# Optimization experiments

Hardware: AMD Instinct MI355X
Metric: run time of the kernel (lower is better)

## Reference

```python
import jax, jax.numpy as jnp
import numpy as np

B, S, DIM = 8, 1, 2048
H = 16
QLR, KVLR = 1536, 512
DN, DR, DV = 128, 64, 128      # qk_nope, qk_rope, v head dims
START = 8191                    # start_pos; end_pos = START + S = 8192
EPS = 1e-6
SCALE = (DN + DR) ** -0.5


def _rms(x, w):
    # F.rms_norm: x / sqrt(mean(x^2)+eps) * w
    return x * w * jax.lax.rsqrt(jnp.mean(jnp.square(x), axis=-1, keepdims=True) + EPS)


def _rope(x, cos, sin):
    # x: [..., r]; consecutive pairs (x0,x1) treated as complex, multiplied by cos+i*sin
    xr, xi = x[..., 0::2], x[..., 1::2]
    out_r = xr * cos - xi * sin
    out_i = xr * sin + xi * cos
    return jnp.stack([out_r, out_i], axis=-1).reshape(x.shape)


def setup_inputs() -> dict:
    key = jax.random.key(0)
    ks = jax.random.split(key, 12)
    # rotary tables for the single decode position
    inv_freq = 1.0 / (10000.0 ** (np.arange(0, DR, 2, dtype=np.float32) / DR))  # [DR/2]
    pos = np.arange(START, START + S, dtype=np.float32)[:, None]                # [S,1]
    ang = pos * inv_freq[None, :]                                               # [S, DR/2]
    return {
        "x": jax.random.normal(ks[0], (B, S, DIM), jnp.float32),
        "start_pos": START,
        "freqs_cos": jnp.asarray(np.cos(ang)),
        "freqs_sin": jnp.asarray(np.sin(ang)),
        "kv_cache_prefix": jax.random.normal(ks[1], (B, START, KVLR), jnp.float32),
        "pe_cache_prefix": jax.random.normal(ks[2], (B, START, DR), jnp.float32),
        "wq_a_w": jax.random.normal(ks[3], (QLR, DIM), jnp.float32) * 0.02,
        "wq_a_b": jnp.zeros((QLR,), jnp.float32),
        "q_norm_w": jnp.ones((QLR,), jnp.float32),
        "wq_b_w": jax.random.normal(ks[4], (H * (DN + DR), QLR), jnp.float32) * 0.02,
        "wq_b_b": jnp.zeros((H * (DN + DR),), jnp.float32),
        "wkv_a_w": jax.random.normal(ks[5], (KVLR + DR, DIM), jnp.float32) * 0.02,
        "wkv_a_b": jnp.zeros((KVLR + DR,), jnp.float32),
        "kv_norm_w": jnp.ones((KVLR,), jnp.float32),
        "wkv_b_w": jax.random.normal(ks[6], (H * (DN + DV), KVLR), jnp.float32) * 0.02,
        "wo_w": jax.random.normal(ks[7], (DIM, H * DV), jnp.float32) * 0.02,
        "wo_b": jnp.zeros((DIM,), jnp.float32),
    }


def reference(x, start_pos, freqs_cos, freqs_sin, kv_cache_prefix, pe_cache_prefix,
              wq_a_w, wq_a_b, q_norm_w, wq_b_w, wq_b_b,
              wkv_a_w, wkv_a_b, kv_norm_w, wkv_b_w, wo_w, wo_b):
    b, s, _ = x.shape
    # low-rank query projection
    q = _rms(x @ wq_a_w.T + wq_a_b, q_norm_w) @ wq_b_w.T + wq_b_b
    q = q.reshape(b, s, H, DN + DR)
    q_nope, q_pe = q[..., :DN], q[..., DN:]
    cos = freqs_cos[None, :, None, :]  # [1,s,1,DR/2]
    sin = freqs_sin[None, :, None, :]
    q_pe = _rope(q_pe, cos, sin)
    # compressed KV + rope key branch
    kvpe = x @ wkv_a_w.T + wkv_a_b               # [b,s,KVLR+DR]
    kv, k_pe = kvpe[..., :KVLR], kvpe[..., KVLR:]
    k_pe = _rope(k_pe[:, :, None, :], cos, sin)[:, :, 0, :]
    # weight absorption: project q_nope into latent space through wkv_b's K-part
    wkv_b = wkv_b_w.reshape(H, DN + DV, KVLR)
    q_abs = jnp.einsum('bshd,hdc->bshc', q_nope, wkv_b[:, :DN])
    # append current step to caches
    kv_cache = jnp.concatenate([kv_cache_prefix, _rms(kv, kv_norm_w)], axis=1)  # [b,t,KVLR]
    pe_cache = jnp.concatenate([pe_cache_prefix, k_pe], axis=1)                 # [b,t,DR]
    # attention in latent space (seqlen=1 decode -> no causal mask needed)
    scores = (jnp.einsum('bshc,btc->bsht', q_abs, kv_cache)
              + jnp.einsum('bshr,btr->bsht', q_pe, pe_cache)) * SCALE
    attn = jax.nn.softmax(scores.astype(jnp.float32), axis=-1).astype(x.dtype)
    out = jnp.einsum('bsht,btc->bshc', attn, kv_cache)
    out = jnp.einsum('bshc,hdc->bshd', out, wkv_b[:, DN:])  # V-part of wkv_b
    return out.reshape(b, s, H * DV) @ wo_w.T + wo_b
```

## Files before the change

kernel.cpp:

```cpp
#include <hip/hip_runtime.h>
#include <math.h>

namespace {
constexpr int B_   = 8;
constexpr int DIM_ = 2048;
constexpr int H_   = 16;
constexpr int QLR_ = 1536;
constexpr int KVLR_= 512;
constexpr int DN_  = 128;
constexpr int DR_  = 64;
constexpr int DV_  = 128;
constexpr int TPRE_= 8191;
constexpr int CE_  = 576;
constexpr int NCH_ = 32;
constexpr int CT_  = 256;
constexpr int TS_  = 32;
constexpr int PSTR_= 20;
constexpr float EPS_ = 1e-6f;
constexpr float SCALE_ = 0.07216878364870322f;

constexpr size_t WS_QLAT  = 0;
constexpr size_t WS_KVPE  = WS_QLAT  + (size_t)B_*QLR_;
constexpr size_t WS_KVNEW = WS_KVPE  + (size_t)B_*CE_;
constexpr size_t WS_PENEW = WS_KVNEW + (size_t)B_*KVLR_;
constexpr size_t WS_QRS   = WS_PENEW + (size_t)B_*DR_;
constexpr size_t WS_QNOPE = WS_QRS   + (size_t)B_;
constexpr size_t WS_QT    = WS_QNOPE + (size_t)B_*H_*DN_;
constexpr size_t WS_MLOC  = WS_QT    + (size_t)B_*CE_*H_;
constexpr size_t WS_LLOC  = WS_MLOC  + (size_t)B_*H_*NCH_;
constexpr size_t WS_OUT2  = WS_LLOC  + (size_t)B_*H_*NCH_;
constexpr size_t WS_OPART = WS_OUT2  + (size_t)B_*DIM_;
}

__device__ __forceinline__ void gload16(const float* src, float* ldsDst) {
  __builtin_amdgcn_global_load_lds((const __attribute__((address_space(1))) void*)src,
                                   (__attribute__((address_space(3))) void*)ldsDst,
                                   16, 0, 0);
}

__device__ __forceinline__ float rsum16(float v) {
  int x = __float_as_int(v);
  v += __int_as_float(__builtin_amdgcn_update_dpp(0, x, 0xB1, 0xF, 0xF, true));
  x = __float_as_int(v);
  v += __int_as_float(__builtin_amdgcn_update_dpp(0, x, 0x4E, 0xF, 0xF, true));
  x = __float_as_int(v);
  v += __int_as_float(__builtin_amdgcn_update_dpp(0, x, 0x141, 0xF, 0xF, true));
  x = __float_as_int(v);
  v += __int_as_float(__builtin_amdgcn_update_dpp(0, x, 0x140, 0xF, 0xF, true));
  return v;
}

__global__ __launch_bounds__(256) void mla_k1(const float* __restrict__ x,
                                              const float* __restrict__ wqa,
                                              const float* __restrict__ bqa,
                                              const float* __restrict__ wkva,
                                              const float* __restrict__ bkva,
                                              float* __restrict__ ws) {
  const int w = threadIdx.x >> 6, l = threadIdx.x & 63;
  const int r = blockIdx.x * 4 + w;
  const float* W; const float* bias; float* out; int rr; int ostride;
  if (r < QLR_) { W = wqa;  bias = bqa;  out = ws + WS_QLAT; rr = r;        ostride = QLR_; }
  else          { W = wkva; bias = bkva; out = ws + WS_KVPE; rr = r - QLR_; ostride = CE_;  }
  const float4* wp = (const float4*)(W + (size_t)rr * DIM_);
  const float4* x4 = (const float4*)x;
  float4 wv[8];
#pragma unroll
  for (int j = 0; j < 8; ++j) wv[j] = wp[l + 64 * j];
  float acc[B_];
#pragma unroll
  for (int b = 0; b < B_; ++b) acc[b] = 0.f;
#pragma unroll
  for (int b = 0; b < B_; ++b) {
#pragma unroll
    for (int j = 0; j < 8; ++j) {
      const float4 xv = x4[b * (DIM_ / 4) + l + 64 * j];
      acc[b] = fmaf(wv[j].x, xv.x, fmaf(wv[j].y, xv.y, fmaf(wv[j].z, xv.z, fmaf(wv[j].w, xv.w, acc[b]))));
    }
  }
#pragma unroll
  for (int b = 0; b < B_; ++b)
#pragma unroll
    for (int s = 32; s; s >>= 1) acc[b] += __shfl_xor(acc[b], s);
  if (l == 0) {
    const float b0 = bias[rr];
#pragma unroll
    for (int b = 0; b < B_; ++b) out[b * ostride + rr] = acc[b] + b0;
  }
}

__global__ __launch_bounds__(256) void mla_k2(const float* __restrict__ kvnw,
                                              const float* __restrict__ fcos,
                                              const float* __restrict__ fsin,
                                              float* __restrict__ ws) {
  const int tid = threadIdx.x;
  const int b = tid >> 5, i = tid & 31;
  const float* kvpe = ws + WS_KVPE + b * CE_;
  float ss = 0.f;
#pragma unroll
  for (int j = 0; j < KVLR_ / 32; ++j) { const float v = kvpe[i + 32 * j]; ss = fmaf(v, v, ss); }
#pragma unroll
  for (int s = 16; s; s >>= 1) ss += __shfl_xor(ss, s, 32);
  const float scale = 1.0f / sqrtf(ss / (float)KVLR_ + EPS_);
  float* kvn = ws + WS_KVNEW + b * KVLR_;
#pragma unroll
  for (int j = 0; j < KVLR_ / 32; ++j) {
    const int c = i + 32 * j;
    kvn[c] = kvpe[c] * kvnw[c] * scale;
  }
  {
    const float xr = kvpe[KVLR_ + 2 * i], xi = kvpe[KVLR_ + 2 * i + 1];
    const float c = fcos[i], s = fsin[i];
    float* pen = ws + WS_PENEW + b * DR_;
    pen[2 * i]     = xr * c - xi * s;
    pen[2 * i + 1] = xr * s + xi * c;
  }
  {
    const float* p = ws + WS_QLAT + b * QLR_;
    float sq = 0.f;
#pragma unroll
    for (int j = 0; j < QLR_ / 32; ++j) { const float v = p[i + 32 * j]; sq = fmaf(v, v, sq); }
#pragma unroll
    for (int s = 16; s; s >>= 1) sq += __shfl_xor(sq, s, 32);
    if (i == 0) ws[WS_QRS + b] = 1.0f / sqrtf(sq / (float)QLR_ + EPS_);
  }
}

__global__ __launch_bounds__(256) void mla_k3(const float* __restrict__ qnw,
                                              const float* __restrict__ wqb,
                                              const float* __restrict__ bqb,
                                              const float* __restrict__ fcos,
                                              const float* __restrict__ fsin,
                                              float* __restrict__ ws) {
  const int w = threadIdx.x >> 6, l = threadIdx.x & 63;
  const int r0 = blockIdx.x * 8 + w * 2;
  const float4* w0p = (const float4*)(wqb + (size_t)r0 * QLR_);
  const float4* w1p = (const float4*)(wqb + (size_t)(r0 + 1) * QLR_);
  const float4* g4  = (const float4*)qnw;
  const float4* x4  = (const float4*)(ws + WS_QLAT);
  float4 wg0[6], wg1[6];
#pragma unroll
  for (int j = 0; j < 6; ++j) {
    const int c4 = l + 64 * j;
    const float4 a = w0p[c4], bb = w1p[c4], g = g4[c4];
    wg0[j].x = a.x * g.x; wg0[j].y = a.y * g.y; wg0[j].z = a.z * g.z; wg0[j].w = a.w * g.w;
    wg1[j].x = bb.x * g.x; wg1[j].y = bb.y * g.y; wg1[j].z = bb.z * g.z; wg1[j].w = bb.w * g.w;
  }
  float acc0[B_], acc1[B_];
#pragma unroll
  for (int b = 0; b < B_; ++b) { acc0[b] = 0.f; acc1[b] = 0.f; }
#pragma unroll
  for (int b = 0; b < B_; ++b) {
#pragma unroll
    for (int j = 0; j < 6; ++j) {
      const float4 xv = x4[b * (QLR_ / 4) + l + 64 * j];
      acc0[b] = fmaf(wg0[j].x, xv.x, fmaf(wg0[j].y, xv.y, fmaf(wg0[j].z, xv.z, fmaf(wg0[j].w, xv.w, acc0[b]))));
      acc1[b] = fmaf(wg1[j].x, xv.x, fmaf(wg1[j].y, xv.y, fmaf(wg1[j].z, xv.z, fmaf(wg1[j].w, xv.w, acc1[b]))));
    }
  }
#pragma unroll
  for (int b = 0; b < B_; ++b)
#pragma unroll
    for (int s = 32; s; s >>= 1) {
      acc0[b] += __shfl_xor(acc0[b], s);
      acc1[b] += __shfl_xor(acc1[b], s);
    }
  if (l == 0) {
    const int h = r0 / (DN_ + DR_);
    const int j0 = r0 - h * (DN_ + DR_);
    const float b0 = bqb[r0], b1 = bqb[r0 + 1];
    if (j0 < DN_) {
      float* qn = ws + WS_QNOPE;
#pragma unroll
      for (int b = 0; b < B_; ++b) {
        const float sb = ws[WS_QRS + b];
        qn[(b * H_ + h) * DN_ + j0]     = acc0[b] * sb + b0;
        qn[(b * H_ + h) * DN_ + j0 + 1] = acc1[b] * sb + b1;
      }
    } else {
      const int i = (j0 - DN_) >> 1;
      const float c = fcos[i], s = fsin[i];
      float* qTT = ws + WS_QT;
#pragma unroll
      for (int b = 0; b < B_; ++b) {
        const float sb = ws[WS_QRS + b];
        const float xr = acc0[b] * sb + b0, xi = acc1[b] * sb + b1;
        qTT[((size_t)(b * H_ + h)) * CE_ + KVLR_ + 2 * i]     = xr * c - xi * s;
        qTT[((size_t)(b * H_ + h)) * CE_ + KVLR_ + 2 * i + 1] = xr * s + xi * c;
      }
    }
  }
}

__global__ __launch_bounds__(256) void mla_k4(const float* __restrict__ wkvb,
                                              float* __restrict__ ws) {
  __shared__ float red[7 * 32 * B_];
  const int h = blockIdx.y;
  const int strip = blockIdx.x;
  const int tid = threadIdx.x;
  const int c = tid & 31, dg = tid >> 5;
  const int cg = strip * 32 + c;
  const float* qn = ws + WS_QNOPE;
  float acc[B_];
#pragma unroll
  for (int b = 0; b < B_; ++b) acc[b] = 0.f;
  const float* wp = wkvb + (size_t)h * 256 * KVLR_ + cg;
#pragma unroll
  for (int dd = 0; dd < 16; ++dd) {
    const int d = dg * 16 + dd;
    const float wv = wp[(size_t)d * KVLR_];
#pragma unroll
    for (int b = 0; b < B_; ++b) acc[b] = fmaf(qn[(b * H_ + h) * DN_ + d], wv, acc[b]);
  }
  if (dg > 0) {
#pragma unroll
    for (int b = 0; b < B_; ++b) red[(((dg - 1) * 32) + c) * B_ + b] = acc[b];
  }
  __syncthreads();
  if (dg == 0) {
    float* qTT = ws + WS_QT;
#pragma unroll
    for (int b = 0; b < B_; ++b) {
      float v = acc[b];
#pragma unroll
      for (int g = 0; g < 7; ++g) v += red[(g * 32 + c) * B_ + b];
      qTT[((size_t)(b * H_ + h)) * CE_ + cg] = v;
    }
  }
}

__global__ __launch_bounds__(512) void mla_k5(const float* __restrict__ kvpre,
                                              const float* __restrict__ pepre,
                                              float* __restrict__ ws) {
  __shared__ float kv_lds[2][TS_ * CE_];
  __shared__ float p_lds[TS_ * PSTR_];
  __shared__ float m_st[H_], l_st[H_], f_st[H_];

  const int b = blockIdx.y, chunk = blockIdx.x;
  const int t0 = chunk * CT_;
  const int tid = threadIdx.x;
  const int w = tid >> 6, l = tid & 63;
  const int cs = l & 15;
  const int hl = l >> 4;
  const int tg = w >> 1;
  const int hg = (w & 1) * 4 + hl;
  const int c4p = tid >> 2, h4p = tid & 3;

  const float* kvnew = ws + WS_KVNEW + b * KVLR_;
  const float* penew = ws + WS_PENEW + b * DR_;

  auto stageKV = [&](float* buf, int s) {
    const int ts0 = t0 + s * TS_;
#pragma unroll
    for (int k = 0; k < 9; ++k) {
      const int i = w + 8 * k;
      const int f = i * 64 + l;
      const int tl = f / 144;
      const int c4 = f - tl * 144;
      const int tgl = ts0 + tl;
      const float* src;
      if (tgl < TPRE_) {
        src = (c4 < 128) ? (kvpre + ((size_t)b * TPRE_ + tgl) * KVLR_ + 4 * c4)
                         : (pepre + ((size_t)b * TPRE_ + tgl) * DR_ + 4 * (c4 - 128));
      } else {
        src = (c4 < 128) ? (kvnew + 4 * c4) : (penew + 4 * (c4 - 128));
      }
      gload16(src, buf + (size_t)i * 64 * 4);
    }
  };

  stageKV(kv_lds[0], 0);

  float4 q0v[9], q1v[9];
  {
    const float* qb0 = ws + WS_QT + ((size_t)(b * H_) + 2 * hg) * CE_ + cs * 36;
    const float* qb1 = qb0 + CE_;
#pragma unroll
    for (int j = 0; j < 9; ++j) {
      q0v[j] = *(const float4*)(qb0 + 4 * j);
      q1v[j] = *(const float4*)(qb1 + 4 * j);
    }
  }
  if (tid < H_) { m_st[tid] = -3.4e38f; l_st[tid] = 0.f; }

  float o[4][4];
#pragma unroll
  for (int cc = 0; cc < 4; ++cc)
#pragma unroll
    for (int hh = 0; hh < 4; ++hh) o[cc][hh] = 0.f;

  for (int s = 0; s < CT_ / TS_; ++s) {
    __syncthreads();
    if (s + 1 < CT_ / TS_) stageKV(kv_lds[(s + 1) & 1], s + 1);
    const float* bufc = kv_lds[s & 1];

    {
      const float* kb = bufc + (tg * 8) * CE_ + cs * 36;
#pragma unroll
      for (int tt = 0; tt < 8; ++tt) {
        const float* kr = kb + tt * CE_;
        float a0 = 0.f, a1 = 0.f;
#pragma unroll
        for (int j = 0; j < 9; ++j) {
          const float4 k = *(const float4*)(kr + 4 * j);
          const float4 qa = q0v[j], qc = q1v[j];
          a0 = fmaf(k.x, qa.x, fmaf(k.y, qa.y, fmaf(k.z, qa.z, fmaf(k.w, qa.w, a0))));
          a1 = fmaf(k.x, qc.x, fmaf(k.y, qc.y, fmaf(k.z, qc.z, fmaf(k.w, qc.w, a1))));
        }
        a0 = rsum16(a0);
        a1 = rsum16(a1);
        if (cs == 0) {
          float2 v; v.x = a0 * SCALE_; v.y = a1 * SCALE_;
          *(float2*)(p_lds + (tg * 8 + tt) * PSTR_ + 2 * hg) = v;
        }
      }
    }
    __syncthreads();

    {
      const int h2 = tid >> 5, tl2 = tid & 31;
      const float sv = p_lds[tl2 * PSTR_ + h2];
      float msub = sv;
#pragma unroll
      for (int d = 16; d; d >>= 1) msub = fmaxf(msub, __shfl_xor(msub, d, 32));
      const float mold = m_st[h2];
      const float mnew = fmaxf(mold, msub);
      const float e = __expf(sv - mnew);
      float lsum = e;
#pragma unroll
      for (int d = 16; d; d >>= 1) lsum += __shfl_xor(lsum, d, 32);
      p_lds[tl2 * PSTR_ + h2] = e;
      if (tl2 == 0) {
        const float fac = __expf(mold - mnew);
        f_st[h2] = fac;
        l_st[h2] = l_st[h2] * fac + lsum;
        m_st[h2] = mnew;
      }
    }
    __syncthreads();

    {
      const float4 fv = *(const float4*)(f_st + 4 * h4p);
#pragma unroll
      for (int cc = 0; cc < 4; ++cc) {
        o[cc][0] *= fv.x; o[cc][1] *= fv.y; o[cc][2] *= fv.z; o[cc][3] *= fv.w;
      }
#pragma unroll 8
      for (int t = 0; t < TS_; ++t) {
        const float4 kq = *(const float4*)(bufc + t * CE_ + 4 * c4p);
        const float4 pq = *(const float4*)(p_lds + t * PSTR_ + 4 * h4p);
        o[0][0] = fmaf(pq.x, kq.x, o[0][0]); o[0][1] = fmaf(pq.y, kq.x, o[0][1]);
        o[0][2] = fmaf(pq.z, kq.x, o[0][2]); o[0][3] = fmaf(pq.w, kq.x, o[0][3]);
        o[1][0] = fmaf(pq.x, kq.y, o[1][0]); o[1][1] = fmaf(pq.y, kq.y, o[1][1]);
        o[1][2] = fmaf(pq.z, kq.y, o[1][2]); o[1][3] = fmaf(pq.w, kq.y, o[1][3]);
        o[2][0] = fmaf(pq.x, kq.z, o[2][0]); o[2][1] = fmaf(pq.y, kq.z, o[2][1]);
        o[2][2] = fmaf(pq.z, kq.z, o[2][2]); o[2][3] = fmaf(pq.w, kq.z, o[2][3]);
        o[3][0] = fmaf(pq.x, kq.w, o[3][0]); o[3][1] = fmaf(pq.y, kq.w, o[3][1]);
        o[3][2] = fmaf(pq.z, kq.w, o[3][2]); o[3][3] = fmaf(pq.w, kq.w, o[3][3]);
      }
    }
  }

  {
    float* Op = ws + WS_OPART;
#pragma unroll
    for (int hh = 0; hh < 4; ++hh) {
      const int h = 4 * h4p + hh;
      float4 v;
      v.x = o[0][hh]; v.y = o[1][hh]; v.z = o[2][hh]; v.w = o[3][hh];
      *(float4*)(Op + ((size_t)(b * H_ + h) * NCH_ + chunk) * KVLR_ + 4 * c4p) = v;
    }
    if (tid < H_) {
      ws[WS_MLOC + (b * H_ + tid) * NCH_ + chunk] = m_st[tid];
      ws[WS_LLOC + (b * H_ + tid) * NCH_ + chunk] = l_st[tid];
    }
  }
}

__global__ __launch_bounds__(256) void mla_k6(const float* __restrict__ wkvb,
                                              float* __restrict__ ws) {
  const int h = blockIdx.x, b = blockIdx.y;
  __shared__ float wgt[NCH_];
  __shared__ float ao[KVLR_];
  __shared__ float Linv;
  const int tid = threadIdx.x;
  if (tid < NCH_) {
    const float m = ws[WS_MLOC + (b * H_ + h) * NCH_ + tid];
    float M = m;
#pragma unroll
    for (int s = 16; s; s >>= 1) M = fmaxf(M, __shfl_xor(M, s, 32));
    const float wv = __expf(m - M);
    wgt[tid] = wv;
    float lv = ws[WS_LLOC + (b * H_ + h) * NCH_ + tid] * wv;
#pragma unroll
    for (int s = 16; s; s >>= 1) lv += __shfl_xor(lv, s, 32);
    if (tid == 0) Linv = 1.0f / lv;
  }
  __syncthreads();
  const float* Ob = ws + WS_OPART + (size_t)(b * H_ + h) * NCH_ * KVLR_;
  float s0 = 0.f, s1 = 0.f;
#pragma unroll 4
  for (int i = 0; i < NCH_; ++i) {
    const float wv = wgt[i];
    s0 = fmaf(wv, Ob[(size_t)i * KVLR_ + tid], s0);
    s1 = fmaf(wv, Ob[(size_t)i * KVLR_ + tid + 256], s1);
  }
  const float li = Linv;
  ao[tid] = s0 * li;
  ao[tid + 256] = s1 * li;
  __syncthreads();
  const int v = tid >> 1, half = tid & 1;
  const float* w2 = wkvb + ((size_t)h * 256 + DN_ + v) * KVLR_ + half * 256;
  const float* a = ao + half * 256;
  float s = 0.f;
#pragma unroll
  for (int c = 0; c < 256; c += 4) {
    const float4 wv = *(const float4*)(w2 + c);
    s = fmaf(wv.x, a[c], s);
    s = fmaf(wv.y, a[c + 1], s);
    s = fmaf(wv.z, a[c + 2], s);
    s = fmaf(wv.w, a[c + 3], s);
  }
  s += __shfl_xor(s, 1);
  if (half == 0) ws[WS_OUT2 + b * DIM_ + h * DV_ + v] = s;
}

__global__ __launch_bounds__(256) void mla_k7(const float* __restrict__ wo,
                                              const float* __restrict__ wob,
                                              const float* __restrict__ ws,
                                              float* __restrict__ out) {
  const int w = threadIdx.x >> 6, l = threadIdx.x & 63;
  const int r = blockIdx.x * 4 + w;
  const float4* wp = (const float4*)(wo + (size_t)r * DIM_);
  const float4* x4 = (const float4*)(ws + WS_OUT2);
  float4 wv[8];
#pragma unroll
  for (int j = 0; j < 8; ++j) wv[j] = wp[l + 64 * j];
  float acc[B_];
#pragma unroll
  for (int b = 0; b < B_; ++b) acc[b] = 0.f;
#pragma unroll
  for (int b = 0; b < B_; ++b) {
#pragma unroll
    for (int j = 0; j < 8; ++j) {
      const float4 xv = x4[b * (DIM_ / 4) + l + 64 * j];
      acc[b] = fmaf(wv[j].x, xv.x, fmaf(wv[j].y, xv.y, fmaf(wv[j].z, xv.z, fmaf(wv[j].w, xv.w, acc[b]))));
    }
  }
#pragma unroll
  for (int b = 0; b < B_; ++b)
#pragma unroll
    for (int s = 32; s; s >>= 1) acc[b] += __shfl_xor(acc[b], s);
  if (l == 0) {
    const float b0 = wob[r];
#pragma unroll
    for (int b = 0; b < B_; ++b) out[b * DIM_ + r] = acc[b] + b0;
  }
}

extern "C" void kernel_launch(void* const* d_in, const int* in_sizes, int n_in,
                              void* d_out, int out_size, void* d_ws, size_t ws_size,
                              hipStream_t stream) {
  (void)in_sizes; (void)n_in; (void)out_size; (void)ws_size;
  const float* x     = (const float*)d_in[0];
  const float* fcos  = (const float*)d_in[2];
  const float* fsin  = (const float*)d_in[3];
  const float* kvpre = (const float*)d_in[4];
  const float* pepre = (const float*)d_in[5];
  const float* wqa   = (const float*)d_in[6];
  const float* bqa   = (const float*)d_in[7];
  const float* qnw   = (const float*)d_in[8];
  const float* wqb   = (const float*)d_in[9];
  const float* bqb   = (const float*)d_in[10];
  const float* wkva  = (const float*)d_in[11];
  const float* bkva  = (const float*)d_in[12];
  const float* kvnw  = (const float*)d_in[13];
  const float* wkvb  = (const float*)d_in[14];
  const float* wo    = (const float*)d_in[15];
  const float* wob   = (const float*)d_in[16];
  float* ws  = (float*)d_ws;
  float* out = (float*)d_out;

  mla_k1<<<dim3((QLR_ + CE_) / 4), dim3(256), 0, stream>>>(x, wqa, bqa, wkva, bkva, ws);
  mla_k2<<<dim3(1), dim3(256), 0, stream>>>(kvnw, fcos, fsin, ws);
  mla_k3<<<dim3(H_ * (DN_ + DR_) / 8), dim3(256), 0, stream>>>(qnw, wqb, bqb, fcos, fsin, ws);
  mla_k4<<<dim3(16, H_), dim3(256), 0, stream>>>(wkvb, ws);
  mla_k5<<<dim3(NCH_, B_), dim3(512), 0, stream>>>(kvpre, pepre, ws);
  mla_k6<<<dim3(H_, B_), dim3(256), 0, stream>>>(wkvb, ws);
  mla_k7<<<dim3(DIM_ / 4), dim3(256), 0, stream>>>(wo, wob, ws, out);
}
```

Measured before the change: 348.3 us.

## Fuse norm stats into first projection, drop k2, two rows per warp in GEMVs

Removes the single-block k2 kernel. k1 now accumulates sum-of-squares for q and kv through atomics, applies rope to k_pe directly, and processes two output rows per warp. The kv RMS normalisation of the new token moves into the attention kernel's last tile, and k3 computes the q rsqrt inline. k6's V-projection is restructured into warp-wide float4 loads with shuffle reductions, and k7 also computes two rows per warp. The cost is a memset launch and atomics, and the two-row GEMVs raise register use.

```diff
diff --git a/kernel.cpp b/kernel.cpp
--- a/kernel.cpp
+++ b/kernel.cpp
@@ -23,8 +23,8 @@
 constexpr size_t WS_KVPE  = WS_QLAT  + (size_t)B_*QLR_;
 constexpr size_t WS_KVNEW = WS_KVPE  + (size_t)B_*CE_;
 constexpr size_t WS_PENEW = WS_KVNEW + (size_t)B_*KVLR_;
-constexpr size_t WS_QRS   = WS_PENEW + (size_t)B_*DR_;
-constexpr size_t WS_QNOPE = WS_QRS   + (size_t)B_;
+constexpr size_t WS_SSQ   = WS_PENEW + (size_t)B_*DR_;
+constexpr size_t WS_QNOPE = WS_SSQ   + 16;
 constexpr size_t WS_QT    = WS_QNOPE + (size_t)B_*H_*DN_;
 constexpr size_t WS_MLOC  = WS_QT    + (size_t)B_*CE_*H_;
 constexpr size_t WS_LLOC  = WS_MLOC  + (size_t)B_*H_*NCH_;
@@ -55,73 +55,80 @@
                                               const float* __restrict__ bqa,
                                               const float* __restrict__ wkva,
                                               const float* __restrict__ bkva,
-                                              float* __restrict__ ws) {
-  const int w = threadIdx.x >> 6, l = threadIdx.x & 63;
-  const int r = blockIdx.x * 4 + w;
-  const float* W; const float* bias; float* out; int rr; int ostride;
-  if (r < QLR_) { W = wqa;  bias = bqa;  out = ws + WS_QLAT; rr = r;        ostride = QLR_; }
-  else          { W = wkva; bias = bkva; out = ws + WS_KVPE; rr = r - QLR_; ostride = CE_;  }
-  const float4* wp = (const float4*)(W + (size_t)rr * DIM_);
-  const float4* x4 = (const float4*)x;
-  float4 wv[8];
-#pragma unroll
-  for (int j = 0; j < 8; ++j) wv[j] = wp[l + 64 * j];
-  float acc[B_];
-#pragma unroll
-  for (int b = 0; b < B_; ++b) acc[b] = 0.f;
-#pragma unroll
-  for (int b = 0; b < B_; ++b) {
-#pragma unroll
-    for (int j = 0; j < 8; ++j) {
-      const float4 xv = x4[b * (DIM_ / 4) + l + 64 * j];
-      acc[b] = fmaf(wv[j].x, xv.x, fmaf(wv[j].y, xv.y, fmaf(wv[j].z, xv.z, fmaf(wv[j].w, xv.w, acc[b]))));
-    }
-  }
-#pragma unroll
-  for (int b = 0; b < B_; ++b)
-#pragma unroll
-    for (int s = 32; s; s >>= 1) acc[b] += __shfl_xor(acc[b], s);
-  if (l == 0) {
-    const float b0 = bias[rr];
-#pragma unroll
-    for (int b = 0; b < B_; ++b) out[b * ostride + rr] = acc[b] + b0;
-  }
-}
-
-__global__ __launch_bounds__(256) void mla_k2(const float* __restrict__ kvnw,
                                               const float* __restrict__ fcos,
                                               const float* __restrict__ fsin,
                                               float* __restrict__ ws) {
-  const int tid = threadIdx.x;
-  const int b = tid >> 5, i = tid & 31;
-  const float* kvpe = ws + WS_KVPE + b * CE_;
-  float ss = 0.f;
-#pragma unroll
-  for (int j = 0; j < KVLR_ / 32; ++j) { const float v = kvpe[i + 32 * j]; ss = fmaf(v, v, ss); }
-#pragma unroll
-  for (int s = 16; s; s >>= 1) ss += __shfl_xor(ss, s, 32);
-  const float scale = 1.0f / sqrtf(ss / (float)KVLR_ + EPS_);
-  float* kvn = ws + WS_KVNEW + b * KVLR_;
-#pragma unroll
-  for (int j = 0; j < KVLR_ / 32; ++j) {
-    const int c = i + 32 * j;
-    kvn[c] = kvpe[c] * kvnw[c] * scale;
-  }
-  {
-    const float xr = kvpe[KVLR_ + 2 * i], xi = kvpe[KVLR_ + 2 * i + 1];
-    const float c = fcos[i], s = fsin[i];
-    float* pen = ws + WS_PENEW + b * DR_;
-    pen[2 * i]     = xr * c - xi * s;
-    pen[2 * i + 1] = xr * s + xi * c;
-  }
-  {
-    const float* p = ws + WS_QLAT + b * QLR_;
-    float sq = 0.f;
-#pragma unroll
-    for (int j = 0; j < QLR_ / 32; ++j) { const float v = p[i + 32 * j]; sq = fmaf(v, v, sq); }
-#pragma unroll
-    for (int s = 16; s; s >>= 1) sq += __shfl_xor(sq, s, 32);
-    if (i == 0) ws[WS_QRS + b] = 1.0f / sqrtf(sq / (float)QLR_ + EPS_);
+  __shared__ float red[4 * B_];
+  const int w = threadIdx.x >> 6, l = threadIdx.x & 63;
+  const int r0 = (blockIdx.x * 4 + w) * 2;
+  const float* W; const float* bias; int rr;
+  if (r0 < QLR_) { W = wqa;  bias = bqa;  rr = r0; }
+  else           { W = wkva; bias = bkva; rr = r0 - QLR_; }
+  const float4* w0p = (const float4*)(W + (size_t)rr * DIM_);
+  const float4* w1p = (const float4*)(W + (size_t)(rr + 1) * DIM_);
+  const float4* x4  = (const float4*)x;
+  float4 wv0[8], wv1[8];
+#pragma unroll
+  for (int j = 0; j < 8; ++j) { wv0[j] = w0p[l + 64 * j]; wv1[j] = w1p[l + 64 * j]; }
+  float acc0[B_], acc1[B_];
+#pragma unroll
+  for (int b = 0; b < B_; ++b) { acc0[b] = 0.f; acc1[b] = 0.f; }
+#pragma unroll
+  for (int b = 0; b < B_; ++b) {
+#pragma unroll
+    for (int j = 0; j < 8; ++j) {
+      const float4 xv = x4[b * (DIM_ / 4) + l + 64 * j];
+      acc0[b] = fmaf(wv0[j].x, xv.x, fmaf(wv0[j].y, xv.y, fmaf(wv0[j].z, xv.z, fmaf(wv0[j].w, xv.w, acc0[b]))));
+      acc1[b] = fmaf(wv1[j].x, xv.x, fmaf(wv1[j].y, xv.y, fmaf(wv1[j].z, xv.z, fmaf(wv1[j].w, xv.w, acc1[b]))));
+    }
+  }
+#pragma unroll
+  for (int b = 0; b < B_; ++b)
+#pragma unroll
+    for (int s = 32; s; s >>= 1) {
+      acc0[b] += __shfl_xor(acc0[b], s);
+      acc1[b] += __shfl_xor(acc1[b], s);
+    }
+  const int rblk = blockIdx.x * 8;
+  if (l == 0) {
+    const float b0 = bias[rr], b1 = bias[rr + 1];
+    if (r0 < QLR_) {
+      float* out = ws + WS_QLAT;
+#pragma unroll
+      for (int b = 0; b < B_; ++b) {
+        const float v0 = acc0[b] + b0, v1 = acc1[b] + b1;
+        out[b * QLR_ + r0]     = v0;
+        out[b * QLR_ + r0 + 1] = v1;
+        red[w * B_ + b] = v0 * v0 + v1 * v1;
+      }
+    } else if (rr < KVLR_) {
+      float* out = ws + WS_KVPE;
+#pragma unroll
+      for (int b = 0; b < B_; ++b) {
+        const float v0 = acc0[b] + b0, v1 = acc1[b] + b1;
+        out[b * CE_ + rr]     = v0;
+        out[b * CE_ + rr + 1] = v1;
+        red[w * B_ + b] = v0 * v0 + v1 * v1;
+      }
+    } else {
+      const int i = (rr - KVLR_) >> 1;
+      const float c = fcos[i], s = fsin[i];
+      float* pen = ws + WS_PENEW;
+#pragma unroll
+      for (int b = 0; b < B_; ++b) {
+        const float xr = acc0[b] + b0, xi = acc1[b] + b1;
+        pen[b * DR_ + 2 * i]     = xr * c - xi * s;
+        pen[b * DR_ + 2 * i + 1] = xr * s + xi * c;
+      }
+    }
+  }
+  if (rblk < QLR_ + KVLR_) {
+    __syncthreads();
+    if (threadIdx.x < B_) {
+      const float sacc = red[0 * B_ + threadIdx.x] + red[1 * B_ + threadIdx.x] +
+                         red[2 * B_ + threadIdx.x] + red[3 * B_ + threadIdx.x];
+      atomicAdd(&ws[WS_SSQ + (rblk >= QLR_ ? B_ : 0) + threadIdx.x], sacc);
+    }
   }
 }
 
@@ -172,7 +179,7 @@
       float* qn = ws + WS_QNOPE;
 #pragma unroll
       for (int b = 0; b < B_; ++b) {
-        const float sb = ws[WS_QRS + b];
+        const float sb = 1.0f / sqrtf(ws[WS_SSQ + b] / (float)QLR_ + EPS_);
         qn[(b * H_ + h) * DN_ + j0]     = acc0[b] * sb + b0;
         qn[(b * H_ + h) * DN_ + j0 + 1] = acc1[b] * sb + b1;
       }
@@ -182,7 +189,7 @@
       float* qTT = ws + WS_QT;
 #pragma unroll
       for (int b = 0; b < B_; ++b) {
-        const float sb = ws[WS_QRS + b];
+        const float sb = 1.0f / sqrtf(ws[WS_SSQ + b] / (float)QLR_ + EPS_);
         const float xr = acc0[b] * sb + b0, xi = acc1[b] * sb + b1;
         qTT[((size_t)(b * H_ + h)) * CE_ + KVLR_ + 2 * i]     = xr * c - xi * s;
         qTT[((size_t)(b * H_ + h)) * CE_ + KVLR_ + 2 * i + 1] = xr * s + xi * c;
@@ -230,6 +237,7 @@
 
 __global__ __launch_bounds__(512) void mla_k5(const float* __restrict__ kvpre,
                                               const float* __restrict__ pepre,
+                                              const float* __restrict__ kvnw,
                                               float* __restrict__ ws) {
   __shared__ float kv_lds[2][TS_ * CE_];
   __shared__ float p_lds[TS_ * PSTR_];
@@ -245,7 +253,7 @@
   const int hg = (w & 1) * 4 + hl;
   const int c4p = tid >> 2, h4p = tid & 3;
 
-  const float* kvnew = ws + WS_KVNEW + b * KVLR_;
+  const float* kvraw = ws + WS_KVPE + b * CE_;
   const float* penew = ws + WS_PENEW + b * DR_;
 
   auto stageKV = [&](float* buf, int s) {
@@ -262,7 +270,7 @@
         src = (c4 < 128) ? (kvpre + ((size_t)b * TPRE_ + tgl) * KVLR_ + 4 * c4)
                          : (pepre + ((size_t)b * TPRE_ + tgl) * DR_ + 4 * (c4 - 128));
       } else {
-        src = (c4 < 128) ? (kvnew + 4 * c4) : (penew + 4 * (c4 - 128));
+        src = (c4 < 128) ? (kvraw + 4 * c4) : (penew + 4 * (c4 - 128));
       }
       gload16(src, buf + (size_t)i * 64 * 4);
     }
@@ -291,7 +299,14 @@
   for (int s = 0; s < CT_ / TS_; ++s) {
     __syncthreads();
     if (s + 1 < CT_ / TS_) stageKV(kv_lds[(s + 1) & 1], s + 1);
-    const float* bufc = kv_lds[s & 1];
+    float* bufc = kv_lds[s & 1];
+
+    if (chunk == NCH_ - 1 && s == CT_ / TS_ - 1) {
+      const float sck = 1.0f / sqrtf(ws[WS_SSQ + B_ + b] / (float)KVLR_ + EPS_);
+      float* row = bufc + (TS_ - 1) * CE_;
+      row[tid] = row[tid] * kvnw[tid] * sck;
+      __syncthreads();
+    }
 
     {
       const float* kb = bufc + (tg * 8) * CE_ + cs * 36;
@@ -408,20 +423,29 @@
   ao[tid] = s0 * li;
   ao[tid + 256] = s1 * li;
   __syncthreads();
-  const int v = tid >> 1, half = tid & 1;
-  const float* w2 = wkvb + ((size_t)h * 256 + DN_ + v) * KVLR_ + half * 256;
-  const float* a = ao + half * 256;
-  float s = 0.f;
-#pragma unroll
-  for (int c = 0; c < 256; c += 4) {
-    const float4 wv = *(const float4*)(w2 + c);
-    s = fmaf(wv.x, a[c], s);
-    s = fmaf(wv.y, a[c + 1], s);
-    s = fmaf(wv.z, a[c + 2], s);
-    s = fmaf(wv.w, a[c + 3], s);
-  }
-  s += __shfl_xor(s, 1);
-  if (half == 0) ws[WS_OUT2 + b * DIM_ + h * DV_ + v] = s;
+
+  const int w6 = tid >> 6, l6 = tid & 63;
+  const float4 ax = *(const float4*)(ao + 4 * l6);
+  const float4 bx = *(const float4*)(ao + 256 + 4 * l6);
+  float* out2 = ws + WS_OUT2 + b * DIM_ + h * DV_;
+#pragma unroll 2
+  for (int k = 0; k < 32; k += 2) {
+    const int v0 = w6 * 32 + k;
+    const float4* w20 = (const float4*)(wkvb + ((size_t)h * 256 + DN_ + v0) * KVLR_);
+    const float4* w21 = (const float4*)(wkvb + ((size_t)h * 256 + DN_ + v0 + 1) * KVLR_);
+    const float4 a0 = w20[l6], c0 = w20[64 + l6];
+    const float4 a1 = w21[l6], c1 = w21[64 + l6];
+    float t0 = fmaf(a0.x, ax.x, fmaf(a0.y, ax.y, fmaf(a0.z, ax.z, fmaf(a0.w, ax.w,
+               fmaf(c0.x, bx.x, fmaf(c0.y, bx.y, fmaf(c0.z, bx.z, c0.w * bx.w)))))));
+    float t1 = fmaf(a1.x, ax.x, fmaf(a1.y, ax.y, fmaf(a1.z, ax.z, fmaf(a1.w, ax.w,
+               fmaf(c1.x, bx.x, fmaf(c1.y, bx.y, fmaf(c1.z, bx.z, c1.w * bx.w)))))));
+#pragma unroll
+    for (int d = 32; d; d >>= 1) {
+      t0 += __shfl_xor(t0, d);
+      t1 += __shfl_xor(t1, d);
+    }
+    if (l6 == 0) { out2[v0] = t0; out2[v0 + 1] = t1; }
+  }
 }
 
 __global__ __launch_bounds__(256) void mla_k7(const float* __restrict__ wo,
@@ -429,31 +453,39 @@
                                               const float* __restrict__ ws,
                                               float* __restrict__ out) {
   const int w = threadIdx.x >> 6, l = threadIdx.x & 63;
-  const int r = blockIdx.x * 4 + w;
-  const float4* wp = (const float4*)(wo + (size_t)r * DIM_);
-  const float4* x4 = (const float4*)(ws + WS_OUT2);
-  float4 wv[8];
-#pragma unroll
-  for (int j = 0; j < 8; ++j) wv[j] = wp[l + 64 * j];
-  float acc[B_];
-#pragma unroll
-  for (int b = 0; b < B_; ++b) acc[b] = 0.f;
+  const int r0 = (blockIdx.x * 4 + w) * 2;
+  const float4* w0p = (const float4*)(wo + (size_t)r0 * DIM_);
+  const float4* w1p = (const float4*)(wo + (size_t)(r0 + 1) * DIM_);
+  const float4* x4  = (const float4*)(ws + WS_OUT2);
+  float4 wv0[8], wv1[8];
+#pragma unroll
+  for (int j = 0; j < 8; ++j) { wv0[j] = w0p[l + 64 * j]; wv1[j] = w1p[l + 64 * j]; }
+  float acc0[B_], acc1[B_];
+#pragma unroll
+  for (int b = 0; b < B_; ++b) { acc0[b] = 0.f; acc1[b] = 0.f; }
 #pragma unroll
   for (int b = 0; b < B_; ++b) {
 #pragma unroll
     for (int j = 0; j < 8; ++j) {
       const float4 xv = x4[b * (DIM_ / 4) + l + 64 * j];
-      acc[b] = fmaf(wv[j].x, xv.x, fmaf(wv[j].y, xv.y, fmaf(wv[j].z, xv.z, fmaf(wv[j].w, xv.w, acc[b]))));
+      acc0[b] = fmaf(wv0[j].x, xv.x, fmaf(wv0[j].y, xv.y, fmaf(wv0[j].z, xv.z, fmaf(wv0[j].w, xv.w, acc0[b]))));
+      acc1[b] = fmaf(wv1[j].x, xv.x, fmaf(wv1[j].y, xv.y, fmaf(wv1[j].z, xv.z, fmaf(wv1[j].w, xv.w, acc1[b]))));
     }
   }
 #pragma unroll
   for (int b = 0; b < B_; ++b)
 #pragma unroll
-    for (int s = 32; s; s >>= 1) acc[b] += __shfl_xor(acc[b], s);
+    for (int s = 32; s; s >>= 1) {
+      acc0[b] += __shfl_xor(acc0[b], s);
+      acc1[b] += __shfl_xor(acc1[b], s);
+    }
   if (l == 0) {
-    const float b0 = wob[r];
-#pragma unroll
-    for (int b = 0; b < B_; ++b) out[b * DIM_ + r] = acc[b] + b0;
+    const float b0 = wob[r0], b1 = wob[r0 + 1];
+#pragma unroll
+    for (int b = 0; b < B_; ++b) {
+      out[b * DIM_ + r0]     = acc0[b] + b0;
+      out[b * DIM_ + r0 + 1] = acc1[b] + b1;
+    }
   }
 }
 
@@ -480,11 +512,11 @@
   float* ws  = (float*)d_ws;
   float* out = (float*)d_out;
 
-  mla_k1<<<dim3((QLR_ + CE_) / 4), dim3(256), 0, stream>>>(x, wqa, bqa, wkva, bkva, ws);
-  mla_k2<<<dim3(1), dim3(256), 0, stream>>>(kvnw, fcos, fsin, ws);
+  hipMemsetAsync((char*)d_ws + WS_SSQ * sizeof(float), 0, 16 * sizeof(float), stream);
+  mla_k1<<<dim3((QLR_ + CE_) / 8), dim3(256), 0, stream>>>(x, wqa, bqa, wkva, bkva, fcos, fsin, ws);
   mla_k3<<<dim3(H_ * (DN_ + DR_) / 8), dim3(256), 0, stream>>>(qnw, wqb, bqb, fcos, fsin, ws);
   mla_k4<<<dim3(16, H_), dim3(256), 0, stream>>>(wkvb, ws);
-  mla_k5<<<dim3(NCH_, B_), dim3(512), 0, stream>>>(kvpre, pepre, ws);
+  mla_k5<<<dim3(NCH_, B_), dim3(512), 0, stream>>>(kvpre, pepre, kvnw, ws);
   mla_k6<<<dim3(H_, B_), dim3(256), 0, stream>>>(wkvb, ws);
-  mla_k7<<<dim3(DIM_ / 4), dim3(256), 0, stream>>>(wo, wob, ws, out);
-}
+  mla_k7<<<dim3(DIM_ / 8), dim3(256), 0, stream>>>(wo, wob, ws, out);
+}
```

New measurement: 351.2 us. About the same (+0.8%).
